# Optimization experiments

Measured on AMD Instinct MI355X. Metric: run time of the kernel, lower is better.

## Reference

```python
import jax, jax.numpy as jnp
import numpy as np

B, IN_DIM, OUT_DIM, MV = 8192, 256, 256, 8


def setup_inputs() -> dict:
    key = jax.random.key(0)
    k1, k2 = jax.random.split(key)
    x = jax.random.normal(k1, (B, IN_DIM, MV), dtype=jnp.float32)
    weights = jax.random.normal(k2, (IN_DIM, OUT_DIM, MV), dtype=jnp.float32) * 0.01
    bias = jnp.zeros((OUT_DIM, MV), dtype=jnp.float32)
    return {"x": x, "weights": weights, "bias": bias}


def reference(x, weights, bias):
    # Simplified GA-3D geometric product, summed over in_dim (j), per out_dim (i):
    #   y[..., i, 0] = sum_j x[..., j, 0]*W[j,i,0] + x[..., j, 1]*W[j,i,1] + x[..., j, 2]*W[j,i,2]
    #   y[..., i, 4] = sum_j x[..., j, 1]*W[j,i,2] - x[..., j, 2]*W[j,i,1] + x[..., j, 4]*W[j,i,0]
    #   all other multivector components receive only the bias.
    # Scalar component: dot over first 3 multivector slots.
    c0 = jnp.einsum('bjk,jik->bi', x[..., 0:3], weights[..., 0:3])  # (B, OUT_DIM)
    # Bivector component e23: x1*w2 - x2*w1 + x4*w0.
    xv = jnp.stack([x[..., 1], -x[..., 2], x[..., 4]], axis=-1)          # (B, IN_DIM, 3)
    wv = jnp.stack([weights[..., 2], weights[..., 1], weights[..., 0]], axis=-1)  # (IN_DIM, OUT_DIM, 3)
    c4 = jnp.einsum('bjk,jik->bi', xv, wv)  # (B, OUT_DIM)
    y = jnp.broadcast_to(bias, (x.shape[0],) + bias.shape)  # (B, OUT_DIM, MV)
    y = y.at[..., 0].add(c0).at[..., 4].add(c4)
    return y
```

## Files before the change

kernel.cpp:

```cpp
#include <hip/hip_runtime.h>
#include <hip/hip_bf16.h>

typedef __attribute__((ext_vector_type(4))) float f32x4;
typedef __attribute__((ext_vector_type(8))) short bf16x8;

#define CS 516

__device__ __forceinline__ short f2bf(float f) {
  __hip_bfloat16 h = __float2bfloat16(f);
  return __builtin_bit_cast(short, h);
}

#define GLD_LDS16(gp, lp)                                                    \
  __builtin_amdgcn_global_load_lds(                                          \
      (const __attribute__((address_space(1))) unsigned int*)(gp),           \
      (__attribute__((address_space(3))) unsigned int*)(lp), 16, 0, 0)

__global__ __launch_bounds__(256) void ga_prep_B(const float* __restrict__ W,
                                                 short* __restrict__ Bp) {
  const int gid = blockIdx.x * 256 + threadIdx.x;
  const int l  = gid & 63;
  const int cg = (gid >> 6) & 31;
  const int it = gid >> 11;
  const int ln = l & 15, q = l >> 4;
  const int hc = cg >> 4;
  const int i  = (cg & 15) * 16 + ln;
  const int j0 = it * 8 + q * 2;
  const float4* W4 = (const float4*)W;

  bf16x8 o;
#pragma unroll
  for (int jj = 0; jj < 2; ++jj) {
    const float4 wv = W4[((j0 + jj) * 256 + i) * 2];
    if (!hc) {
      o[jj * 4 + 0] = f2bf(wv.x); o[jj * 4 + 1] = f2bf(wv.y);
      o[jj * 4 + 2] = f2bf(wv.z); o[jj * 4 + 3] = 0;
    } else {
      o[jj * 4 + 0] = 0;           o[jj * 4 + 1] = f2bf(wv.z);
      o[jj * 4 + 2] = f2bf(-wv.y); o[jj * 4 + 3] = f2bf(wv.x);
    }
  }
  *(bf16x8*)&Bp[(size_t)gid * 8] = o;
}

__global__ __launch_bounds__(256) void ga_prep_A(const float* __restrict__ x,
                                                 short* __restrict__ A) {
  const int g = blockIdx.x * 256 + threadIdx.x;
  const int row = g >> 7, rem = g & 127;
  const int q = rem >> 5, c = rem & 31;
  const int cp = c ^ ((row & 7) << 2);
  const float4* x4 = (const float4*)x + (size_t)(row * 256 + q * 64 + c * 2) * 2;
  const float4 a0 = x4[0], a1 = x4[1], b0 = x4[2], b1 = x4[3];
  bf16x8 o;
  o[0] = f2bf(a0.x); o[1] = f2bf(a0.y); o[2] = f2bf(a0.z); o[3] = f2bf(a1.x);
  o[4] = f2bf(b0.x); o[5] = f2bf(b0.y); o[6] = f2bf(b0.z); o[7] = f2bf(b1.x);
  *(bf16x8*)&A[((size_t)row * 128 + q * 32 + cp) * 8] = o;
}

__global__ __launch_bounds__(1024, 4) void ga_mv_main(
    const short* __restrict__ A, const short* __restrict__ Bp,
    const float* __restrict__ bias, float* __restrict__ y) {
  __shared__ __align__(16) char smem[65536];
  short* lds_s = (short*)smem;
  float* c_lds = (float*)smem;

  const int t = threadIdx.x;
  const int bm = blockIdx.x;
  const int lane = t & 63, w = t >> 6;
  const int ln = lane & 15, qq = lane >> 4, lnl = lane & 7;
  const int R0 = bm * 32;

  const short* asrc = A + ((size_t)(R0 + (t >> 5)) * 128 + (t & 31)) * 8;
#pragma unroll
  for (int q = 0; q < 4; ++q)
    GLD_LDS16(asrc + q * 256, lds_s + q * 8192 + t * 8);

  const size_t bbase = (size_t)w * 1024 + lane * 8;
  bf16x8 Bf[4][2];
#define LB(itv, b)                                                           \
  {                                                                          \
    const short* p = Bp + (size_t)(itv) * 16384 + bbase;                     \
    Bf[b][0] = *(const bf16x8*)(p);                                          \
    Bf[b][1] = *(const bf16x8*)(p + 512);                                    \
  }
  LB(0, 0);
  LB(1, 1);
  LB(2, 2);
  LB(3, 3);

  __syncthreads();

  f32x4 acc[2][2] = {};
  const int abase = ln * 256 + qq * 8;
#pragma unroll
  for (int it = 0; it < 32; ++it) {
    const int q = it >> 3, tau = it & 7;
    const short* Aq = lds_s + q * 8192 + abase + ((tau ^ lnl) << 5);
    const bf16x8 af0 = *(const bf16x8*)Aq;
    const bf16x8 af1 = *(const bf16x8*)(Aq + 4096);
#pragma unroll
    for (int n = 0; n < 2; ++n) {
      acc[0][n] = __builtin_amdgcn_mfma_f32_16x16x32_bf16(af0, Bf[it & 3][n],
                                                          acc[0][n], 0, 0, 0);
      acc[1][n] = __builtin_amdgcn_mfma_f32_16x16x32_bf16(af1, Bf[it & 3][n],
                                                          acc[1][n], 0, 0, 0);
    }
    if (it + 4 < 32) LB(it + 4, it & 3);
  }
  __syncthreads();

  const int h = t & 1, p = (t >> 1) & 255, rh = t >> 9;
  const float4 bv = ((const float4*)bias)[p * 2 + h];
  f32x4* y4 = (f32x4*)y;

#pragma unroll
  for (int ep = 0; ep < 2; ++ep) {
    if (ep) __syncthreads();
#pragma unroll
    for (int n = 0; n < 2; ++n)
#pragma unroll
      for (int r = 0; r < 4; ++r)
        c_lds[(qq * 4 + r) * CS + w * 32 + n * 16 + ln] = acc[ep][n][r];
    __syncthreads();
#pragma unroll
    for (int rr = 0; rr < 8; ++rr) {
      const int row = rr * 2 + rh;
      f32x4 o;
      o[0] = bv.x; o[1] = bv.y; o[2] = bv.z; o[3] = bv.w;
      o[0] += c_lds[row * CS + h * 256 + p];
      __builtin_nontemporal_store(
          o, &y4[((size_t)(R0 + ep * 16 + row) * 256 + p) * 2 + h]);
    }
  }
}

extern "C" void kernel_launch(void* const* d_in, const int* in_sizes, int n_in,
                              void* d_out, int out_size, void* d_ws, size_t ws_size,
                              hipStream_t stream) {
  const float* x = (const float*)d_in[0];
  const float* W = (const float*)d_in[1];
  const float* bias = (const float*)d_in[2];
  float* y = (float*)d_out;
  short* Bp = (short*)d_ws;
  short* A = (short*)d_ws + (1 << 19);

  ga_prep_B<<<dim3(256), dim3(256), 0, stream>>>(W, Bp);
  ga_prep_A<<<dim3(4096), dim3(256), 0, stream>>>(x, A);
  ga_mv_main<<<dim3(256), dim3(1024), 0, stream>>>(A, Bp, bias, y);
}
```

Before: 133.4 us.

## Fuse x bf16 conversion into main GEMM with triple-buffered async fp32 loads

```diff
diff --git a/kernel.cpp b/kernel.cpp
--- a/kernel.cpp
+++ b/kernel.cpp
@@ -3,7 +3,10 @@
 
 typedef __attribute__((ext_vector_type(4))) float f32x4;
 typedef __attribute__((ext_vector_type(8))) short bf16x8;
-
+typedef __attribute__((ext_vector_type(4))) short short4v;
+
+#define XCH 16384
+#define ACH 136
 #define CS 516
 
 __device__ __forceinline__ short f2bf(float f) {
@@ -15,6 +18,24 @@
   __builtin_amdgcn_global_load_lds(                                          \
       (const __attribute__((address_space(1))) unsigned int*)(gp),           \
       (__attribute__((address_space(3))) unsigned int*)(lp), 16, 0, 0)
+
+#define WAITV(N)                                            \
+  {                                                         \
+    asm volatile("s_waitcnt vmcnt(" #N ")" ::: "memory");   \
+    __builtin_amdgcn_sched_barrier(0);                      \
+  }
+#define BAR()                                               \
+  {                                                         \
+    __builtin_amdgcn_s_barrier();                           \
+    __builtin_amdgcn_sched_barrier(0);                      \
+  }
+#define QBAR()                                              \
+  {                                                         \
+    asm volatile("s_waitcnt lgkmcnt(0)" ::: "memory");      \
+    __builtin_amdgcn_sched_barrier(0);                      \
+    __builtin_amdgcn_s_barrier();                           \
+    __builtin_amdgcn_sched_barrier(0);                      \
+  }
 
 __global__ __launch_bounds__(256) void ga_prep_B(const float* __restrict__ W,
                                                  short* __restrict__ Bp) {
@@ -43,70 +64,103 @@
   *(bf16x8*)&Bp[(size_t)gid * 8] = o;
 }
 
-__global__ __launch_bounds__(256) void ga_prep_A(const float* __restrict__ x,
-                                                 short* __restrict__ A) {
-  const int g = blockIdx.x * 256 + threadIdx.x;
-  const int row = g >> 7, rem = g & 127;
-  const int q = rem >> 5, c = rem & 31;
-  const int cp = c ^ ((row & 7) << 2);
-  const float4* x4 = (const float4*)x + (size_t)(row * 256 + q * 64 + c * 2) * 2;
-  const float4 a0 = x4[0], a1 = x4[1], b0 = x4[2], b1 = x4[3];
-  bf16x8 o;
-  o[0] = f2bf(a0.x); o[1] = f2bf(a0.y); o[2] = f2bf(a0.z); o[3] = f2bf(a1.x);
-  o[4] = f2bf(b0.x); o[5] = f2bf(b0.y); o[6] = f2bf(b0.z); o[7] = f2bf(b1.x);
-  *(bf16x8*)&A[((size_t)row * 128 + q * 32 + cp) * 8] = o;
-}
-
 __global__ __launch_bounds__(1024, 4) void ga_mv_main(
-    const short* __restrict__ A, const short* __restrict__ Bp,
+    const float* __restrict__ x, const short* __restrict__ Bp,
     const float* __restrict__ bias, float* __restrict__ y) {
-  __shared__ __align__(16) char smem[65536];
-  short* lds_s = (short*)smem;
+  __shared__ __align__(16) char smem[107008];
+  short* xb0 = (short*)smem;
+  short* xb1 = (short*)smem + XCH;
+  short* xb2 = (short*)smem + 2 * XCH;
+  short* Ab  = (short*)smem + 3 * XCH;
   float* c_lds = (float*)smem;
 
   const int t = threadIdx.x;
-  const int bm = blockIdx.x;
   const int lane = t & 63, w = t >> 6;
-  const int ln = lane & 15, qq = lane >> 4, lnl = lane & 7;
-  const int R0 = bm * 32;
-
-  const short* asrc = A + ((size_t)(R0 + (t >> 5)) * 128 + (t & 31)) * 8;
-#pragma unroll
-  for (int q = 0; q < 4; ++q)
-    GLD_LDS16(asrc + q * 256, lds_s + q * 8192 + t * 8);
+  const int ln = lane & 15, qq = lane >> 4;
+  const int R0 = blockIdx.x * 32;
+
+  const float* xs0 = x + (size_t)(R0 + w) * 2048 + (lane >> 1) * 8 + (lane & 1) * 4;
+  const float* xs1 = x + (size_t)(R0 + 16 + w) * 2048 + (lane >> 1) * 8 + (lane & 1) * 4;
+  const int xd0 = w * 512 + lane * 8;
+  const int xd1 = (16 + w) * 512 + lane * 8;
+
+#define XB(c) ((c) % 3 == 0 ? xb0 : ((c) % 3 == 1 ? xb1 : xb2))
+#define GLDC(c)                                  \
+  {                                              \
+    GLD_LDS16(xs0 + (c) * 256, XB(c) + xd0);     \
+    GLD_LDS16(xs1 + (c) * 256, XB(c) + xd1);     \
+  }
+
+  const int prow = t >> 5, pj = t & 31;
+#define PROCC(c)                                                       \
+  {                                                                    \
+    const float* xp = (const float*)XB(c) + prow * 256 + pj * 8;       \
+    const f32x4 v = *(const f32x4*)xp;                                 \
+    const float v4 = xp[4];                                            \
+    short4v a;                                                         \
+    a[0] = f2bf(v[0]); a[1] = f2bf(v[1]);                              \
+    a[2] = f2bf(v[2]); a[3] = f2bf(v4);                                \
+    *(short4v*)&Ab[prow * ACH + pj * 4] = a;                           \
+  }
 
   const size_t bbase = (size_t)w * 1024 + lane * 8;
   bf16x8 Bf[4][2];
-#define LB(itv, b)                                                           \
-  {                                                                          \
-    const short* p = Bp + (size_t)(itv) * 16384 + bbase;                     \
-    Bf[b][0] = *(const bf16x8*)(p);                                          \
-    Bf[b][1] = *(const bf16x8*)(p + 512);                                    \
-  }
+#define LB(itv, b)                                                     \
+  {                                                                    \
+    const short* p = Bp + (size_t)(itv) * 16384 + bbase;               \
+    Bf[b][0] = *(const bf16x8*)(p);                                    \
+    Bf[b][1] = *(const bf16x8*)(p + 512);                              \
+  }
+
+  f32x4 acc[2][2] = {};
+
+#define MFMAC(c)                                                              \
+  {                                                                           \
+    _Pragma("unroll")                                                         \
+    for (int tau = 0; tau < 4; ++tau) {                                       \
+      const int it = (c) * 4 + tau;                                           \
+      const bf16x8 af0 =                                                      \
+          *(const bf16x8*)&Ab[ln * ACH + (tau * 8 + qq * 2) * 4];             \
+      const bf16x8 af1 =                                                      \
+          *(const bf16x8*)&Ab[(16 + ln) * ACH + (tau * 8 + qq * 2) * 4];      \
+      _Pragma("unroll")                                                       \
+      for (int n = 0; n < 2; ++n) {                                           \
+        acc[0][n] = __builtin_amdgcn_mfma_f32_16x16x32_bf16(af0, Bf[it & 3][n], \
+                                                            acc[0][n], 0, 0, 0); \
+        acc[1][n] = __builtin_amdgcn_mfma_f32_16x16x32_bf16(af1, Bf[it & 3][n], \
+                                                            acc[1][n], 0, 0, 0); \
+      }                                                                       \
+      if (it + 4 < 32) LB(it + 4, it & 3);                                    \
+    }                                                                         \
+  }
+
+  GLDC(0);
+  GLDC(1);
+  GLDC(2);
   LB(0, 0);
   LB(1, 1);
   LB(2, 2);
   LB(3, 3);
 
-  __syncthreads();
-
-  f32x4 acc[2][2] = {};
-  const int abase = ln * 256 + qq * 8;
-#pragma unroll
-  for (int it = 0; it < 32; ++it) {
-    const int q = it >> 3, tau = it & 7;
-    const short* Aq = lds_s + q * 8192 + abase + ((tau ^ lnl) << 5);
-    const bf16x8 af0 = *(const bf16x8*)Aq;
-    const bf16x8 af1 = *(const bf16x8*)(Aq + 4096);
-#pragma unroll
-    for (int n = 0; n < 2; ++n) {
-      acc[0][n] = __builtin_amdgcn_mfma_f32_16x16x32_bf16(af0, Bf[it & 3][n],
-                                                          acc[0][n], 0, 0, 0);
-      acc[1][n] = __builtin_amdgcn_mfma_f32_16x16x32_bf16(af1, Bf[it & 3][n],
-                                                          acc[1][n], 0, 0, 0);
-    }
-    if (it + 4 < 32) LB(it + 4, it & 3);
-  }
+#define CHUNK(c, Wc)               \
+  {                                \
+    WAITV(Wc);                     \
+    BAR();                         \
+    PROCC(c);                      \
+    QBAR();                        \
+    if ((c) + 3 < 8) GLDC((c) + 3); \
+    MFMAC(c);                      \
+  }
+
+  CHUNK(0, 12)
+  CHUNK(1, 20)
+  CHUNK(2, 28)
+  CHUNK(3, 28)
+  CHUNK(4, 28)
+  CHUNK(5, 28)
+  CHUNK(6, 26)
+  CHUNK(7, 24)
+
   __syncthreads();
 
   const int h = t & 1, p = (t >> 1) & 255, rh = t >> 9;
@@ -142,9 +196,7 @@
   const float* bias = (const float*)d_in[2];
   float* y = (float*)d_out;
   short* Bp = (short*)d_ws;
-  short* A = (short*)d_ws + (1 << 19);
 
   ga_prep_B<<<dim3(256), dim3(256), 0, stream>>>(W, Bp);
-  ga_prep_A<<<dim3(4096), dim3(256), 0, stream>>>(x, A);
-  ga_mv_main<<<dim3(256), dim3(1024), 0, stream>>>(A, Bp, bias, y);
-}
+  ga_mv_main<<<dim3(256), dim3(1024), 0, stream>>>(x, Bp, bias, y);
+}
```

Result: faster. 129.9 us (-2.6%).

## Fuse x bf16 conversion into main kernel with double-buffered LDS staging

Applied to the files above, without the earlier changes.

```diff
diff --git a/kernel.cpp b/kernel.cpp
--- a/kernel.cpp
+++ b/kernel.cpp
@@ -3,7 +3,11 @@
 
 typedef __attribute__((ext_vector_type(4))) float f32x4;
 typedef __attribute__((ext_vector_type(8))) short bf16x8;
+typedef __attribute__((ext_vector_type(4))) short short4v;
 
+#define ACH2 1048
+#define AB_BYTES 67072
+#define XB_OFF(b) (AB_BYTES + (b) * 32768)
 #define CS 516
 
 __device__ __forceinline__ short f2bf(float f) {
@@ -15,6 +19,24 @@
   __builtin_amdgcn_global_load_lds(                                          \
       (const __attribute__((address_space(1))) unsigned int*)(gp),           \
       (__attribute__((address_space(3))) unsigned int*)(lp), 16, 0, 0)
+
+#define WAITV(N)                                            \
+  {                                                         \
+    asm volatile("s_waitcnt vmcnt(" #N ")" ::: "memory");   \
+    __builtin_amdgcn_sched_barrier(0);                      \
+  }
+#define BAR()                                               \
+  {                                                         \
+    __builtin_amdgcn_s_barrier();                           \
+    __builtin_amdgcn_sched_barrier(0);                      \
+  }
+#define QBAR()                                              \
+  {                                                         \
+    asm volatile("s_waitcnt lgkmcnt(0)" ::: "memory");      \
+    __builtin_amdgcn_sched_barrier(0);                      \
+    __builtin_amdgcn_s_barrier();                           \
+    __builtin_amdgcn_sched_barrier(0);                      \
+  }
 
 __global__ __launch_bounds__(256) void ga_prep_B(const float* __restrict__ W,
                                                  short* __restrict__ Bp) {
@@ -43,61 +65,76 @@
   *(bf16x8*)&Bp[(size_t)gid * 8] = o;
 }
 
-__global__ __launch_bounds__(256) void ga_prep_A(const float* __restrict__ x,
-                                                 short* __restrict__ A) {
-  const int g = blockIdx.x * 256 + threadIdx.x;
-  const int row = g >> 7, rem = g & 127;
-  const int q = rem >> 5, c = rem & 31;
-  const int cp = c ^ ((row & 7) << 2);
-  const float4* x4 = (const float4*)x + (size_t)(row * 256 + q * 64 + c * 2) * 2;
-  const float4 a0 = x4[0], a1 = x4[1], b0 = x4[2], b1 = x4[3];
-  bf16x8 o;
-  o[0] = f2bf(a0.x); o[1] = f2bf(a0.y); o[2] = f2bf(a0.z); o[3] = f2bf(a1.x);
-  o[4] = f2bf(b0.x); o[5] = f2bf(b0.y); o[6] = f2bf(b0.z); o[7] = f2bf(b1.x);
-  *(bf16x8*)&A[((size_t)row * 128 + q * 32 + cp) * 8] = o;
-}
-
 __global__ __launch_bounds__(1024, 4) void ga_mv_main(
-    const short* __restrict__ A, const short* __restrict__ Bp,
+    const float* __restrict__ x, const short* __restrict__ Bp,
     const float* __restrict__ bias, float* __restrict__ y) {
-  __shared__ __align__(16) char smem[65536];
-  short* lds_s = (short*)smem;
-  float* c_lds = (float*)smem;
+  __shared__ __align__(16) char smem[132608];
+  short* Ab = (short*)smem;
+  float* c_lds = (float*)(smem + AB_BYTES);
 
   const int t = threadIdx.x;
-  const int bm = blockIdx.x;
   const int lane = t & 63, w = t >> 6;
-  const int ln = lane & 15, qq = lane >> 4, lnl = lane & 7;
-  const int R0 = bm * 32;
+  const int ln = lane & 15, qq = lane >> 4;
+  const int R0 = blockIdx.x * 32;
 
-  const short* asrc = A + ((size_t)(R0 + (t >> 5)) * 128 + (t & 31)) * 8;
-#pragma unroll
-  for (int q = 0; q < 4; ++q)
-    GLD_LDS16(asrc + q * 256, lds_s + q * 8192 + t * 8);
+  const float* xsrc =
+      x + (size_t)(R0 + (w >> 2)) * 2048 + ((w & 3) * 128 + lane) * 4;
+  const int xdst = (w >> 2) * 4096 + (w & 3) * 1024 + lane * 8;
+
+#define GLDX(s)                                                  \
+  {                                                              \
+    const float* gp = xsrc + (s) * 8192;                         \
+    short* lp = (short*)(smem + XB_OFF((s)&1)) + xdst;           \
+    GLD_LDS16(gp, lp);                                           \
+    GLD_LDS16(gp + 256, lp + 512);                               \
+  }
+
+  const int srow = t >> 8, cj = t & 255;
+#define CONV(s)                                                              \
+  {                                                                          \
+    const float* xp =                                                        \
+        (const float*)(smem + XB_OFF((s)&1)) + srow * 2048 + cj * 8;         \
+    const f32x4 v = *(const f32x4*)xp;                                       \
+    const float v4 = xp[4];                                                  \
+    short4v a;                                                               \
+    a[0] = f2bf(v[0]); a[1] = f2bf(v[1]);                                    \
+    a[2] = f2bf(v[2]); a[3] = f2bf(v4);                                      \
+    *(short4v*)&Ab[(4 * (s) + srow) * ACH2 + cj * 4] = a;                    \
+  }
+
+#define SUBSTEP(s, Wc)             \
+  {                                \
+    WAITV(Wc);                     \
+    BAR();                         \
+    CONV(s);                       \
+    QBAR();                        \
+    if ((s) + 2 < 8) GLDX((s) + 2); \
+  }
+
+  GLDX(0);
+  GLDX(1);
+  SUBSTEP(0, 2) SUBSTEP(1, 2) SUBSTEP(2, 2) SUBSTEP(3, 2)
+  SUBSTEP(4, 2) SUBSTEP(5, 2) SUBSTEP(6, 2) SUBSTEP(7, 0)
 
   const size_t bbase = (size_t)w * 1024 + lane * 8;
   bf16x8 Bf[4][2];
-#define LB(itv, b)                                                           \
-  {                                                                          \
-    const short* p = Bp + (size_t)(itv) * 16384 + bbase;                     \
-    Bf[b][0] = *(const bf16x8*)(p);                                          \
-    Bf[b][1] = *(const bf16x8*)(p + 512);                                    \
+#define LB(itv, b)                                                     \
+  {                                                                    \
+    const short* p = Bp + (size_t)(itv) * 16384 + bbase;               \
+    Bf[b][0] = *(const bf16x8*)(p);                                    \
+    Bf[b][1] = *(const bf16x8*)(p + 512);                              \
   }
   LB(0, 0);
   LB(1, 1);
   LB(2, 2);
   LB(3, 3);
 
-  __syncthreads();
-
   f32x4 acc[2][2] = {};
-  const int abase = ln * 256 + qq * 8;
 #pragma unroll
   for (int it = 0; it < 32; ++it) {
-    const int q = it >> 3, tau = it & 7;
-    const short* Aq = lds_s + q * 8192 + abase + ((tau ^ lnl) << 5);
-    const bf16x8 af0 = *(const bf16x8*)Aq;
-    const bf16x8 af1 = *(const bf16x8*)(Aq + 4096);
+    const int jo = (it * 8 + qq * 2) * 4;
+    const bf16x8 af0 = *(const bf16x8*)&Ab[ln * ACH2 + jo];
+    const bf16x8 af1 = *(const bf16x8*)&Ab[(16 + ln) * ACH2 + jo];
 #pragma unroll
     for (int n = 0; n < 2; ++n) {
       acc[0][n] = __builtin_amdgcn_mfma_f32_16x16x32_bf16(af0, Bf[it & 3][n],
@@ -107,7 +144,6 @@
     }
     if (it + 4 < 32) LB(it + 4, it & 3);
   }
-  __syncthreads();
 
   const int h = t & 1, p = (t >> 1) & 255, rh = t >> 9;
   const float4 bv = ((const float4*)bias)[p * 2 + h];
@@ -115,13 +151,13 @@
 
 #pragma unroll
   for (int ep = 0; ep < 2; ++ep) {
-    if (ep) __syncthreads();
+    if (ep) QBAR();
 #pragma unroll
     for (int n = 0; n < 2; ++n)
 #pragma unroll
       for (int r = 0; r < 4; ++r)
         c_lds[(qq * 4 + r) * CS + w * 32 + n * 16 + ln] = acc[ep][n][r];
-    __syncthreads();
+    QBAR();
 #pragma unroll
     for (int rr = 0; rr < 8; ++rr) {
       const int row = rr * 2 + rh;
@@ -142,9 +178,7 @@
   const float* bias = (const float*)d_in[2];
   float* y = (float*)d_out;
   short* Bp = (short*)d_ws;
-  short* A = (short*)d_ws + (1 << 19);
 
   ga_prep_B<<<dim3(256), dim3(256), 0, stream>>>(W, Bp);
-  ga_prep_A<<<dim3(4096), dim3(256), 0, stream>>>(x, A);
-  ga_mv_main<<<dim3(256), dim3(1024), 0, stream>>>(A, Bp, bias, y);
+  ga_mv_main<<<dim3(256), dim3(1024), 0, stream>>>(x, Bp, bias, y);
 }
```

Result: faster. 124.2 us (-6.9%).

## Derive bivector weight fragment in registers and drop LDS staging in GEMM

Applied to the files above, without the earlier changes.

```diff
diff --git a/kernel.cpp b/kernel.cpp
--- a/kernel.cpp
+++ b/kernel.cpp
@@ -2,29 +2,22 @@
 #include <hip/hip_bf16.h>
 
 typedef __attribute__((ext_vector_type(4))) float f32x4;
+typedef __attribute__((ext_vector_type(4))) unsigned int u32x4;
 typedef __attribute__((ext_vector_type(8))) short bf16x8;
-
-#define CS 516
 
 __device__ __forceinline__ short f2bf(float f) {
   __hip_bfloat16 h = __float2bfloat16(f);
   return __builtin_bit_cast(short, h);
 }
 
-#define GLD_LDS16(gp, lp)                                                    \
-  __builtin_amdgcn_global_load_lds(                                          \
-      (const __attribute__((address_space(1))) unsigned int*)(gp),           \
-      (__attribute__((address_space(3))) unsigned int*)(lp), 16, 0, 0)
-
 __global__ __launch_bounds__(256) void ga_prep_B(const float* __restrict__ W,
                                                  short* __restrict__ Bp) {
   const int gid = blockIdx.x * 256 + threadIdx.x;
   const int l  = gid & 63;
-  const int cg = (gid >> 6) & 31;
-  const int it = gid >> 11;
+  const int cg = (gid >> 6) & 15;
+  const int it = gid >> 10;
   const int ln = l & 15, q = l >> 4;
-  const int hc = cg >> 4;
-  const int i  = (cg & 15) * 16 + ln;
+  const int i  = cg * 16 + ln;
   const int j0 = it * 8 + q * 2;
   const float4* W4 = (const float4*)W;
 
@@ -32,13 +25,8 @@
 #pragma unroll
   for (int jj = 0; jj < 2; ++jj) {
     const float4 wv = W4[((j0 + jj) * 256 + i) * 2];
-    if (!hc) {
-      o[jj * 4 + 0] = f2bf(wv.x); o[jj * 4 + 1] = f2bf(wv.y);
-      o[jj * 4 + 2] = f2bf(wv.z); o[jj * 4 + 3] = 0;
-    } else {
-      o[jj * 4 + 0] = 0;           o[jj * 4 + 1] = f2bf(wv.z);
-      o[jj * 4 + 2] = f2bf(-wv.y); o[jj * 4 + 3] = f2bf(wv.x);
-    }
+    o[jj * 4 + 0] = f2bf(wv.x); o[jj * 4 + 1] = f2bf(wv.y);
+    o[jj * 4 + 2] = f2bf(wv.z); o[jj * 4 + 3] = 0;
   }
   *(bf16x8*)&Bp[(size_t)gid * 8] = o;
 }
@@ -46,91 +34,59 @@
 __global__ __launch_bounds__(256) void ga_prep_A(const float* __restrict__ x,
                                                  short* __restrict__ A) {
   const int g = blockIdx.x * 256 + threadIdx.x;
-  const int row = g >> 7, rem = g & 127;
-  const int q = rem >> 5, c = rem & 31;
-  const int cp = c ^ ((row & 7) << 2);
-  const float4* x4 = (const float4*)x + (size_t)(row * 256 + q * 64 + c * 2) * 2;
-  const float4 a0 = x4[0], a1 = x4[1], b0 = x4[2], b1 = x4[3];
+  const float4* xp = (const float4*)x + (size_t)g * 4;
+  const float4 a0 = xp[0], a1 = xp[1], b0 = xp[2], b1 = xp[3];
   bf16x8 o;
   o[0] = f2bf(a0.x); o[1] = f2bf(a0.y); o[2] = f2bf(a0.z); o[3] = f2bf(a1.x);
   o[4] = f2bf(b0.x); o[5] = f2bf(b0.y); o[6] = f2bf(b0.z); o[7] = f2bf(b1.x);
-  *(bf16x8*)&A[((size_t)row * 128 + q * 32 + cp) * 8] = o;
+  *(bf16x8*)&A[(size_t)g * 8] = o;
 }
 
-__global__ __launch_bounds__(1024, 4) void ga_mv_main(
+__global__ __launch_bounds__(256, 6) void ga_gemm(
     const short* __restrict__ A, const short* __restrict__ Bp,
     const float* __restrict__ bias, float* __restrict__ y) {
-  __shared__ __align__(16) char smem[65536];
-  short* lds_s = (short*)smem;
-  float* c_lds = (float*)smem;
+  const int t = threadIdx.x, lane = t & 63, w = t >> 6;
+  const int ln = lane & 15, qq = lane >> 4;
+  const int bm = blockIdx.x >> 2, cb = blockIdx.x & 3;
+  const int R0 = bm * 16, cg = cb * 4 + w;
+  const int i = cg * 16 + ln;
 
-  const int t = threadIdx.x;
-  const int bm = blockIdx.x;
-  const int lane = t & 63, w = t >> 6;
-  const int ln = lane & 15, qq = lane >> 4, lnl = lane & 7;
-  const int R0 = bm * 32;
+  const short* ap = A + (size_t)(R0 + ln) * 1024 + qq * 8;
+  const short* bp = Bp + (size_t)cg * 512 + lane * 8;
 
-  const short* asrc = A + ((size_t)(R0 + (t >> 5)) * 128 + (t & 31)) * 8;
-#pragma unroll
-  for (int q = 0; q < 4; ++q)
-    GLD_LDS16(asrc + q * 256, lds_s + q * 8192 + t * 8);
+  bf16x8 Af[4], Bf[4];
+#define LA(it, b) { Af[b] = *(const bf16x8*)(ap + (it) * 32); }
+#define LB(it, b) { Bf[b] = *(const bf16x8*)(bp + (size_t)(it) * 8192); }
+  LA(0, 0) LA(1, 1) LA(2, 2) LA(3, 3)
+  LB(0, 0) LB(1, 1) LB(2, 2) LB(3, 3)
 
-  const size_t bbase = (size_t)w * 1024 + lane * 8;
-  bf16x8 Bf[4][2];
-#define LB(itv, b)                                                           \
-  {                                                                          \
-    const short* p = Bp + (size_t)(itv) * 16384 + bbase;                     \
-    Bf[b][0] = *(const bf16x8*)(p);                                          \
-    Bf[b][1] = *(const bf16x8*)(p + 512);                                    \
-  }
-  LB(0, 0);
-  LB(1, 1);
-  LB(2, 2);
-  LB(3, 3);
-
-  __syncthreads();
-
-  f32x4 acc[2][2] = {};
-  const int abase = ln * 256 + qq * 8;
+  f32x4 acc0 = {}, acc1 = {};
 #pragma unroll
   for (int it = 0; it < 32; ++it) {
-    const int q = it >> 3, tau = it & 7;
-    const short* Aq = lds_s + q * 8192 + abase + ((tau ^ lnl) << 5);
-    const bf16x8 af0 = *(const bf16x8*)Aq;
-    const bf16x8 af1 = *(const bf16x8*)(Aq + 4096);
+    const bf16x8 af = Af[it & 3];
+    const bf16x8 F = Bf[it & 3];
+    const u32x4 fu = __builtin_bit_cast(u32x4, F);
+    u32x4 gu;
+    gu.x = fu.y << 16;
+    gu.y = ((fu.x >> 16) | (fu.x << 16)) ^ 0x8000u;
+    gu.z = fu.w << 16;
+    gu.w = ((fu.z >> 16) | (fu.z << 16)) ^ 0x8000u;
+    const bf16x8 G = __builtin_bit_cast(bf16x8, gu);
+    acc0 = __builtin_amdgcn_mfma_f32_16x16x32_bf16(af, F, acc0, 0, 0, 0);
+    acc1 = __builtin_amdgcn_mfma_f32_16x16x32_bf16(af, G, acc1, 0, 0, 0);
+    if (it + 4 < 32) { LA(it + 4, it & 3) LB(it + 4, it & 3) }
+  }
+
+  const f32x4 bv0 = ((const f32x4*)bias)[i * 2];
+  const f32x4 bv1 = ((const f32x4*)bias)[i * 2 + 1];
+  f32x4* yp = (f32x4*)y + ((size_t)(R0 + qq * 4) * 256 + i) * 2;
 #pragma unroll
-    for (int n = 0; n < 2; ++n) {
-      acc[0][n] = __builtin_amdgcn_mfma_f32_16x16x32_bf16(af0, Bf[it & 3][n],
-                                                          acc[0][n], 0, 0, 0);
-      acc[1][n] = __builtin_amdgcn_mfma_f32_16x16x32_bf16(af1, Bf[it & 3][n],
-                                                          acc[1][n], 0, 0, 0);
-    }
-    if (it + 4 < 32) LB(it + 4, it & 3);
-  }
-  __syncthreads();
-
-  const int h = t & 1, p = (t >> 1) & 255, rh = t >> 9;
-  const float4 bv = ((const float4*)bias)[p * 2 + h];
-  f32x4* y4 = (f32x4*)y;
-
-#pragma unroll
-  for (int ep = 0; ep < 2; ++ep) {
-    if (ep) __syncthreads();
-#pragma unroll
-    for (int n = 0; n < 2; ++n)
-#pragma unroll
-      for (int r = 0; r < 4; ++r)
-        c_lds[(qq * 4 + r) * CS + w * 32 + n * 16 + ln] = acc[ep][n][r];
-    __syncthreads();
-#pragma unroll
-    for (int rr = 0; rr < 8; ++rr) {
-      const int row = rr * 2 + rh;
-      f32x4 o;
-      o[0] = bv.x; o[1] = bv.y; o[2] = bv.z; o[3] = bv.w;
-      o[0] += c_lds[row * CS + h * 256 + p];
-      __builtin_nontemporal_store(
-          o, &y4[((size_t)(R0 + ep * 16 + row) * 256 + p) * 2 + h]);
-    }
+  for (int r = 0; r < 4; ++r) {
+    f32x4 o0 = bv0, o1 = bv1;
+    o0[0] += acc0[r];
+    o1[0] += acc1[r];
+    __builtin_nontemporal_store(o0, yp + (size_t)r * 512);
+    __builtin_nontemporal_store(o1, yp + (size_t)r * 512 + 1);
   }
 }
 
@@ -142,9 +98,9 @@
   const float* bias = (const float*)d_in[2];
   float* y = (float*)d_out;
   short* Bp = (short*)d_ws;
-  short* A = (short*)d_ws + (1 << 19);
+  short* A = (short*)d_ws + (1 << 18);
 
-  ga_prep_B<<<dim3(256), dim3(256), 0, stream>>>(W, Bp);
+  ga_prep_B<<<dim3(128), dim3(256), 0, stream>>>(W, Bp);
   ga_prep_A<<<dim3(4096), dim3(256), 0, stream>>>(x, A);
-  ga_mv_main<<<dim3(256), dim3(1024), 0, stream>>>(A, Bp, bias, y);
+  ga_gemm<<<dim3(2048), dim3(256), 0, stream>>>(A, Bp, bias, y);
 }
```

New measurement: 154.2 us. 15.7% more time.
